# Performance work log

Measured on AMD Instinct MI355X. Metric: run time of the kernel, lower is better.

## Reference

```python
import jax, jax.numpy as jnp
import numpy as np

NUM_HEADS = 8

def setup_inputs() -> dict:
    key = jax.random.key(0)
    ks = jax.random.split(key, 5)
    b, c, h, w = 8, 512, 32, 32
    sd = 1.0 / np.sqrt(c)
    x = jax.random.normal(ks[0], (b, c, h, w), dtype=jnp.float32)
    Wq = jax.random.normal(ks[1], (c, c), dtype=jnp.float32) * sd
    Wk = jax.random.normal(ks[2], (c, c), dtype=jnp.float32) * sd
    Wv = jax.random.normal(ks[3], (c, c), dtype=jnp.float32) * sd
    Wo = jax.random.normal(ks[4], (c, c), dtype=jnp.float32) * sd
    z = jnp.zeros((c,), dtype=jnp.float32)
    return {"x": x, "Wq": Wq, "bq": z, "Wk": Wk, "bk": z, "Wv": Wv, "bv": z, "Wo": Wo, "bo": z}

def reference(x, Wq, bq, Wk, bk, Wv, bv, Wo, bo):
    b, c, h, w = x.shape
    nh = NUM_HEADS
    hd = c // nh
    # [b, c, h, w] -> [b, h*w, c]
    xr = jnp.transpose(x, (0, 2, 3, 1)).reshape(b, h * w, c)
    def proj(W, bias):
        y = xr @ W.T + bias
        return y.reshape(b, h * w, nh, hd)
    q = proj(Wq, bq)  # [b, s, nh, hd]
    k = proj(Wk, bk)
    v = proj(Wv, bv)
    scale = 1.0 / np.sqrt(hd)
    att = jnp.einsum("bsnd,btnd->bnst", q, k) * scale  # [b, nh, s, s]
    att = jax.nn.softmax(att, axis=-1)
    # dropout is identity in eval mode
    out = jnp.einsum("bnst,btnd->bsnd", att, v).reshape(b, h, w, c)
    out = out @ Wo.T + bo  # [b, h, w, c]
    return out
```

## Files before the change

### kernel.cpp

```cpp
#include <hip/hip_runtime.h>

typedef _Float16 half_t;
typedef _Float16 half2v __attribute__((ext_vector_type(2)));
typedef _Float16 half8 __attribute__((ext_vector_type(8)));
typedef float f32x4 __attribute__((ext_vector_type(4)));

static_assert(sizeof(half8) == 16, "half8 must be 16B");

__device__ inline half8 make_h8(unsigned long lo, unsigned long hi) {
  union { half8 v; unsigned long u[2]; } x;
  x.u[0] = lo; x.u[1] = hi;
  return x.v;
}

__device__ inline float fast_exp2(float x) {
#if __has_builtin(__builtin_amdgcn_exp2f)
  return __builtin_amdgcn_exp2f(x);
#else
  return exp2f(x);
#endif
}

__device__ inline half2v cvt_pk_f16(float lo, float hi) {
  return __builtin_bit_cast(half2v, __builtin_amdgcn_cvt_pkrtz(lo, hi));
}

__device__ inline void gload_lds16(const void* g, void* l) {
  __builtin_amdgcn_global_load_lds(
      (const __attribute__((address_space(1))) unsigned int*)g,
      (__attribute__((address_space(3))) unsigned int*)l, 16, 0, 0);
}

__global__ void prep_x_kernel(const float* __restrict__ x, half_t* __restrict__ xr) {
  __shared__ float t[32][33];
  const int b = blockIdx.z;
  const int c0 = blockIdx.y * 32;
  const int s0 = blockIdx.x * 32;
  const int tx = threadIdx.x, ty = threadIdx.y;
  const float* xp = x + ((size_t)b * 512 + c0) * 1024 + s0;
#pragma unroll
  for (int r = 0; r < 4; r++) {
    const int cl = ty + 8 * r;
    t[cl][tx] = xp[(size_t)cl * 1024 + tx];
  }
  __syncthreads();
  half_t* op = xr + ((size_t)b * 1024 + s0) * 512 + c0;
#pragma unroll
  for (int r = 0; r < 4; r++) {
    const int sl = ty + 8 * r;
    op[(size_t)sl * 512 + tx] = (half_t)t[tx][sl];
  }
}

__global__ void prep_w_kernel(const float* __restrict__ w0, const float* __restrict__ w1,
                              const float* __restrict__ w2, const float* __restrict__ w3,
                              half_t* __restrict__ out) {
  const int mz = blockIdx.y;
  const float* src = (mz == 0) ? w0 : (mz == 1) ? w1 : (mz == 2) ? w2 : w3;
  const int i = blockIdx.x * 256 + threadIdx.x;
  const float4 v = ((const float4*)src)[i];
  half_t* o = out + (size_t)mz * 262144 + (size_t)i * 4;
  o[0] = (half_t)v.x; o[1] = (half_t)v.y; o[2] = (half_t)v.z; o[3] = (half_t)v.w;
}

template <int MODE, int BM>
__global__ __launch_bounds__(256, 2) void gemm_kernel(
    const half_t* __restrict__ A, const half_t* __restrict__ Wall,
    const float* __restrict__ b0, const float* __restrict__ b1,
    const float* __restrict__ b2, half_t* __restrict__ qkv,
    float* __restrict__ fout) {
  constexpr int K = 512;
  constexpr int IREP = BM / 32;
  __shared__ alignas(16) half_t lA[BM * 64];
  __shared__ alignas(16) half_t lB[128 * 64];

  const int z = blockIdx.z;
  const half_t* W = Wall + (size_t)z * K * 512;
  const float* bias = (MODE == 1) ? b0 : (z == 0 ? b0 : (z == 1 ? b1 : b2));

  const int tid = threadIdx.x;
  const int lane = tid & 63;
  const int wid = tid >> 6;
  const int wm = wid >> 1, wn = wid & 1;
  const int g = lane >> 4, r16 = lane & 15;
  const int m0 = blockIdx.y * BM, n0 = blockIdx.x * 128;

  f32x4 acc[IREP][4];
#pragma unroll
  for (int i = 0; i < IREP; i++)
#pragma unroll
    for (int j = 0; j < 4; j++) acc[i][j] = (f32x4){0.f, 0.f, 0.f, 0.f};

  for (int k0 = 0; k0 < K; k0 += 64) {
#pragma unroll
    for (int t = 0; t < BM / 32; t++) {
      const int o = (t * 256 + tid) * 16;
      const int row = o >> 7;
      const int kbs = (o & 127) ^ ((row & 7) << 4);
      gload_lds16((const char*)(A + (size_t)(m0 + row) * K + k0) + kbs, (char*)lA + o);
    }
#pragma unroll
    for (int t = 0; t < 4; t++) {
      const int o = (t * 256 + tid) * 16;
      const int row = o >> 7;
      const int kbs = (o & 127) ^ ((row & 7) << 4);
      gload_lds16((const char*)(W + (size_t)(n0 + row) * K + k0) + kbs, (char*)lB + o);
    }
    __syncthreads();
#pragma unroll
    for (int kk = 0; kk < 2; kk++) {
      half8 af[IREP], bf[4];
#pragma unroll
      for (int i = 0; i < IREP; i++) {
        const int row = wm * (BM / 2) + i * 16 + r16;
        const int sw = (row & 7) << 4;
        const char* p = (const char*)lA + row * 128;
        af[i] = make_h8(*(const unsigned long*)(p + ((kk * 64 + g * 8) ^ sw)),
                        *(const unsigned long*)(p + ((kk * 64 + 32 + g * 8) ^ sw)));
      }
#pragma unroll
      for (int j = 0; j < 4; j++) {
        const int row = wn * 64 + j * 16 + r16;
        const int sw = (row & 7) << 4;
        const char* p = (const char*)lB + row * 128;
        bf[j] = make_h8(*(const unsigned long*)(p + ((kk * 64 + g * 8) ^ sw)),
                        *(const unsigned long*)(p + ((kk * 64 + 32 + g * 8) ^ sw)));
      }
#pragma unroll
      for (int i = 0; i < IREP; i++)
#pragma unroll
        for (int j = 0; j < 4; j++)
          acc[i][j] = __builtin_amdgcn_mfma_f32_16x16x32_f16(af[i], bf[j], acc[i][j], 0, 0, 0);
    }
    __syncthreads();
  }

  half_t* dst = (MODE == 0) ? (qkv + (size_t)z * 4194304) : (half_t*)nullptr;
  const float scale = (MODE == 0 && z == 0) ? 0.18033688011112042f : 1.0f;
#pragma unroll
  for (int i = 0; i < IREP; i++) {
#pragma unroll
    for (int j = 0; j < 4; j++) {
      const int n = n0 + wn * 64 + j * 16 + r16;
      const float bvv = bias[n];
      const int mb = m0 + wm * (BM / 2) + i * 16 + g * 4;
      if (MODE == 0 && z == 2) {
        const int bb = mb >> 10, s0v = mb & 1023, hh = n >> 6, d = n & 63;
        const int kvb = s0v & 31;
        const int sp0 = (s0v & ~31) | ((((kvb & 15) >> 2) << 3) + ((kvb >> 4) << 2));
        half_t* dp = dst + (size_t)(bb * 8 + hh) * 65536 + ((size_t)d << 10) + sp0;
        union { half_t e[4]; unsigned long u; } st;
#pragma unroll
        for (int rr = 0; rr < 4; rr++) st.e[rr] = (half_t)(acc[i][j][rr] + bvv);
        *(unsigned long*)dp = st.u;
      } else {
#pragma unroll
        for (int rr = 0; rr < 4; rr++) {
          const int m = mb + rr;
          const float v = (acc[i][j][rr] + bvv) * scale;
          if (MODE == 0) {
            const int bb = m >> 10, s = m & 1023, hh = n >> 6, d = n & 63;
            dst[(((size_t)(bb * 8 + hh) * 1024 + s) << 6) + d] = (half_t)v;
          } else {
            fout[(size_t)m * 512 + n] = v;
          }
        }
      }
    }
  }
}


__device__ inline half8 lds_frag128(const half_t* l, int row, int cb) {
  const char* p = (const char*)l + row * 128 + (cb ^ ((row & 7) << 4));
  return *(const half8*)p;
}

__global__ __launch_bounds__(256) void attn_kernel(
    const half_t* __restrict__ Q, const half_t* __restrict__ Kh,
    const half_t* __restrict__ V, half_t* __restrict__ O) {
  __shared__ alignas(16) half_t lK[2][64 * 64];
  __shared__ alignas(16) half_t lV[2][64 * 64];

  const int tid = threadIdx.x;
  const int lane = tid & 63;
  const int w = tid >> 6;
  const int bh = blockIdx.y, b = bh >> 3, h = bh & 7;
  const int g = lane >> 4, r16 = lane & 15;
  const size_t base = (size_t)bh * 65536;
  const half_t* Qp = Q + base;
  const half_t* Kp = Kh + base;
  const half_t* Vt = V + base;
  const int q0 = blockIdx.x * 128 + w * 32;

  half8 qf[2][2];
#pragma unroll
  for (int qt = 0; qt < 2; qt++) {
    const half_t* qrow = Qp + (size_t)(q0 + qt * 16 + r16) * 64 + g * 8;
    qf[qt][0] = *(const half8*)(qrow);
    qf[qt][1] = *(const half8*)(qrow + 32);
  }

  f32x4 acc[2][4];
#pragma unroll
  for (int qt = 0; qt < 2; qt++)
#pragma unroll
    for (int i = 0; i < 4; i++) acc[qt][i] = (f32x4){0.f, 0.f, 0.f, 0.f};
  float lsum[2] = {0.f, 0.f};

  auto stage = [&](int kv0, int bufi) {
    half_t* lk = lK[bufi];
    half_t* lv = lV[bufi];
    const char* ksrc = (const char*)(Kp + (size_t)kv0 * 64);
    const char* vsrc = (const char*)Vt + (size_t)kv0 * 2;
#pragma unroll
    for (int i = 0; i < 2; i++) {
      const int o = i * 4096 + tid * 16;
      const int row = o >> 7;
      const int cs = (o & 127) ^ ((row & 7) << 4);
      gload_lds16(ksrc + row * 128 + cs, (char*)lk + o);
      gload_lds16(vsrc + row * 2048 + cs, (char*)lv + o);
    }
  };

  stage(0, 0);
  __syncthreads();

  int buf = 0;
  for (int kv0 = 0; kv0 < 1024; kv0 += 64) {
    if (kv0 + 64 < 1024) stage(kv0 + 64, buf ^ 1);
    const half_t* lk = lK[buf];
    const half_t* lv = lV[buf];
#pragma unroll
    for (int sub = 0; sub < 2; sub++) {
      half8 kf0 = lds_frag128(lk, sub * 32 + r16, g * 16);
      half8 kf1 = lds_frag128(lk, sub * 32 + r16, 64 + g * 16);
      half8 kf2 = lds_frag128(lk, sub * 32 + 16 + r16, g * 16);
      half8 kf3 = lds_frag128(lk, sub * 32 + 16 + r16, 64 + g * 16);
      half8 vf[4];
#pragma unroll
      for (int dt = 0; dt < 4; dt++)
        vf[dt] = lds_frag128(lv, dt * 16 + r16, sub * 64 + g * 16);

#pragma unroll
      for (int qt = 0; qt < 2; qt++) {
        f32x4 s0 = {0.f, 0.f, 0.f, 0.f}, s1 = {0.f, 0.f, 0.f, 0.f};
        __builtin_amdgcn_s_setprio(1);
        s0 = __builtin_amdgcn_mfma_f32_16x16x32_f16(kf0, qf[qt][0], s0, 0, 0, 0);
        s0 = __builtin_amdgcn_mfma_f32_16x16x32_f16(kf1, qf[qt][1], s0, 0, 0, 0);
        s1 = __builtin_amdgcn_mfma_f32_16x16x32_f16(kf2, qf[qt][0], s1, 0, 0, 0);
        s1 = __builtin_amdgcn_mfma_f32_16x16x32_f16(kf3, qf[qt][1], s1, 0, 0, 0);
        __builtin_amdgcn_s_setprio(0);

        float p[8];
#pragma unroll
        for (int i = 0; i < 4; i++) { p[i] = fast_exp2(s0[i]); p[4 + i] = fast_exp2(s1[i]); }
        lsum[qt] += ((p[0] + p[1]) + (p[2] + p[3])) + ((p[4] + p[5]) + (p[6] + p[7]));

        union { half8 v; half2v h2[4]; } pu;
#pragma unroll
        for (int i = 0; i < 4; i++)
          pu.h2[i] = cvt_pk_f16(p[2 * i], p[2 * i + 1]);
        __builtin_amdgcn_s_setprio(1);
#pragma unroll
        for (int dt = 0; dt < 4; dt++)
          acc[qt][dt] = __builtin_amdgcn_mfma_f32_16x16x32_f16(vf[dt], pu.v, acc[qt][dt], 0, 0, 0);
        __builtin_amdgcn_s_setprio(0);
      }
    }
    __syncthreads();
    buf ^= 1;
  }

#pragma unroll
  for (int qt = 0; qt < 2; qt++) {
    float l = lsum[qt];
    l += __shfl_xor(l, 16);
    l += __shfl_xor(l, 32);
    const float inv = 1.f / l;
    half_t* orow = O + ((size_t)b * 1024 + q0 + qt * 16 + r16) * 512 + h * 64;
#pragma unroll
    for (int dt = 0; dt < 4; dt++) {
      union { half_t e[4]; unsigned long u; } st;
#pragma unroll
      for (int rr = 0; rr < 4; rr++) st.e[rr] = (half_t)(acc[qt][dt][rr] * inv);
      *(unsigned long*)(orow + dt * 16 + g * 4) = st.u;
    }
  }
}

extern "C" void kernel_launch(void* const* d_in, const int* in_sizes, int n_in,
                              void* d_out, int out_size, void* d_ws, size_t ws_size,
                              hipStream_t stream) {
  if (ws_size < 44040192u) return;
  const float* x  = (const float*)d_in[0];
  const float* Wq = (const float*)d_in[1];
  const float* bq = (const float*)d_in[2];
  const float* Wk = (const float*)d_in[3];
  const float* bk = (const float*)d_in[4];
  const float* Wv = (const float*)d_in[5];
  const float* bv = (const float*)d_in[6];
  const float* Wo = (const float*)d_in[7];
  const float* bo = (const float*)d_in[8];
  char* ws = (char*)d_ws;
  half_t* xr = (half_t*)(ws + 0);
  half_t* W4 = (half_t*)(ws + 8388608);
  half_t* Qb = (half_t*)(ws + 10485760);
  half_t* AO = (half_t*)(ws + 35651584);
  float* out = (float*)d_out;

  prep_x_kernel<<<dim3(32, 16, 8), dim3(32, 8), 0, stream>>>(x, xr);
  prep_w_kernel<<<dim3(256, 4), 256, 0, stream>>>(Wq, Wk, Wv, Wo, W4);
  gemm_kernel<0, 128><<<dim3(4, 64, 3), 256, 0, stream>>>(xr, W4, bq, bk, bv, Qb, nullptr);
  attn_kernel<<<dim3(8, 64), 256, 0, stream>>>(Qb, Qb + 4194304, Qb + 8388608, AO);
  gemm_kernel<1, 64><<<dim3(4, 128, 1), 256, 0, stream>>>(AO, W4 + 786432, bo, nullptr, nullptr,
                                                          nullptr, out);
}
```

Baseline: 77.04 us.

## Merge prep kernels and remap block indices for XCD-local L2 reuse

Merges the x-transpose and weight-conversion prep kernels into one launch, using an extra z-slice of blocks for the weights, which removes one kernel launch. It also remaps flat block IDs in the GEMM and attention kernels so that blocks sharing the same A rows or the same batch-head land on the same XCD (round-robin dispatch over 8 XCDs). The aim is better L2 hit rates for shared K/V and weight tiles. The remapping relies on the hardware's round-robin dispatch order and changes which blocks run concurrently.

```diff
diff --git a/kernel.cpp b/kernel.cpp
--- a/kernel.cpp
+++ b/kernel.cpp
@@ -31,36 +31,45 @@
       (__attribute__((address_space(3))) unsigned int*)l, 16, 0, 0);
 }
 
-__global__ void prep_x_kernel(const float* __restrict__ x, half_t* __restrict__ xr) {
-  __shared__ float t[32][33];
-  const int b = blockIdx.z;
-  const int c0 = blockIdx.y * 32;
-  const int s0 = blockIdx.x * 32;
-  const int tx = threadIdx.x, ty = threadIdx.y;
-  const float* xp = x + ((size_t)b * 512 + c0) * 1024 + s0;
-#pragma unroll
-  for (int r = 0; r < 4; r++) {
-    const int cl = ty + 8 * r;
-    t[cl][tx] = xp[(size_t)cl * 1024 + tx];
-  }
-  __syncthreads();
-  half_t* op = xr + ((size_t)b * 1024 + s0) * 512 + c0;
-#pragma unroll
-  for (int r = 0; r < 4; r++) {
-    const int sl = ty + 8 * r;
-    op[(size_t)sl * 512 + tx] = (half_t)t[tx][sl];
-  }
-}
-
-__global__ void prep_w_kernel(const float* __restrict__ w0, const float* __restrict__ w1,
-                              const float* __restrict__ w2, const float* __restrict__ w3,
-                              half_t* __restrict__ out) {
-  const int mz = blockIdx.y;
-  const float* src = (mz == 0) ? w0 : (mz == 1) ? w1 : (mz == 2) ? w2 : w3;
-  const int i = blockIdx.x * 256 + threadIdx.x;
-  const float4 v = ((const float4*)src)[i];
-  half_t* o = out + (size_t)mz * 262144 + (size_t)i * 4;
-  o[0] = (half_t)v.x; o[1] = (half_t)v.y; o[2] = (half_t)v.z; o[3] = (half_t)v.w;
+__global__ void prep_kernel(const float* __restrict__ x,
+                            const float* __restrict__ w0, const float* __restrict__ w1,
+                            const float* __restrict__ w2, const float* __restrict__ w3,
+                            half_t* __restrict__ xr, half_t* __restrict__ wout) {
+  if (blockIdx.z < 8) {
+    __shared__ float t[32][33];
+    const int b = blockIdx.z;
+    const int c0 = blockIdx.y * 32;
+    const int s0 = blockIdx.x * 32;
+    const int tx = threadIdx.x, ty = threadIdx.y;
+    const float* xp = x + ((size_t)b * 512 + c0) * 1024 + s0;
+#pragma unroll
+    for (int r = 0; r < 4; r++) {
+      const int cl = ty + 8 * r;
+      t[cl][tx] = xp[(size_t)cl * 1024 + tx];
+    }
+    __syncthreads();
+    half_t* op = xr + ((size_t)b * 1024 + s0) * 512 + c0;
+#pragma unroll
+    for (int r = 0; r < 4; r++) {
+      const int sl = ty + 8 * r;
+      op[(size_t)sl * 512 + tx] = (half_t)t[tx][sl];
+    }
+  } else {
+    const int f = blockIdx.x + 32 * blockIdx.y;
+    const int tid = threadIdx.x + 32 * threadIdx.y;
+    const int base = (f * 256 + tid) * 2;
+#pragma unroll
+    for (int r = 0; r < 2; r++) {
+      const int i = base + r;
+      const int mz = i >> 16;
+      const float* src = (mz == 0) ? w0 : (mz == 1) ? w1 : (mz == 2) ? w2 : w3;
+      const float4 v = ((const float4*)src)[i & 65535];
+      union { half_t e[4]; unsigned long u; } st;
+      st.e[0] = (half_t)v.x; st.e[1] = (half_t)v.y;
+      st.e[2] = (half_t)v.z; st.e[3] = (half_t)v.w;
+      *(unsigned long*)(wout + (size_t)i * 4) = st.u;
+    }
+  }
 }
 
 template <int MODE, int BM>
@@ -74,7 +83,19 @@
   __shared__ alignas(16) half_t lA[BM * 64];
   __shared__ alignas(16) half_t lB[128 * 64];
 
-  const int z = blockIdx.z;
+  int bx, by, bz;
+  {
+    const int flat = blockIdx.x + gridDim.x * (blockIdx.y + gridDim.y * blockIdx.z);
+    const int xcd = flat & 7;
+    const int r = flat >> 3;
+    if (MODE == 0) {
+      bx = r & 3; bz = (r >> 2) % 3; by = (r / 12) * 8 + xcd;
+    } else {
+      bx = r & 3; bz = 0; by = (r >> 2) * 8 + xcd;
+    }
+  }
+
+  const int z = bz;
   const half_t* W = Wall + (size_t)z * K * 512;
   const float* bias = (MODE == 1) ? b0 : (z == 0 ? b0 : (z == 1 ? b1 : b2));
 
@@ -83,7 +104,7 @@
   const int wid = tid >> 6;
   const int wm = wid >> 1, wn = wid & 1;
   const int g = lane >> 4, r16 = lane & 15;
-  const int m0 = blockIdx.y * BM, n0 = blockIdx.x * 128;
+  const int m0 = by * BM, n0 = bx * 128;
 
   f32x4 acc[IREP][4];
 #pragma unroll
@@ -185,13 +206,18 @@
   const int tid = threadIdx.x;
   const int lane = tid & 63;
   const int w = tid >> 6;
-  const int bh = blockIdx.y, b = bh >> 3, h = bh & 7;
+  const int flat = blockIdx.x + (blockIdx.y << 3);
+  const int xcd = flat & 7;
+  const int tt = flat >> 3;
+  const int qch = tt & 7;
+  const int bh = ((tt >> 3) << 3) | xcd;
+  const int b = bh >> 3, h = bh & 7;
   const int g = lane >> 4, r16 = lane & 15;
   const size_t base = (size_t)bh * 65536;
   const half_t* Qp = Q + base;
   const half_t* Kp = Kh + base;
   const half_t* Vt = V + base;
-  const int q0 = blockIdx.x * 128 + w * 32;
+  const int q0 = qch * 128 + w * 32;
 
   half8 qf[2][2];
 #pragma unroll
@@ -309,8 +335,7 @@
   half_t* AO = (half_t*)(ws + 35651584);
   float* out = (float*)d_out;
 
-  prep_x_kernel<<<dim3(32, 16, 8), dim3(32, 8), 0, stream>>>(x, xr);
-  prep_w_kernel<<<dim3(256, 4), 256, 0, stream>>>(Wq, Wk, Wv, Wo, W4);
+  prep_kernel<<<dim3(32, 16, 9), dim3(32, 8), 0, stream>>>(x, Wq, Wk, Wv, Wo, xr, W4);
   gemm_kernel<0, 128><<<dim3(4, 64, 3), 256, 0, stream>>>(xr, W4, bq, bk, bv, Qb, nullptr);
   attn_kernel<<<dim3(8, 64), 256, 0, stream>>>(Qb, Qb + 4194304, Qb + 8388608, AO);
   gemm_kernel<1, 64><<<dim3(4, 128, 1), 256, 0, stream>>>(AO, W4 + 786432, bo, nullptr, nullptr,
```

Result: faster. 70.55 us (-8.4%).
